# Kernel optimization log

Measured on AMD Instinct MI355X. Metric: run time of the kernel, lower is better.

Reference implementation:

```python
import jax, jax.numpy as jnp
import numpy as np

GROUPS = 32
NUM_HEADS = 4
EPS = 1e-5


def setup_inputs() -> dict:
    key = jax.random.key(0)
    ks = jax.random.split(key, 3)
    B, C, H, W = 16, 256, 32, 32
    x = jax.random.normal(ks[0], (B, C, H, W), dtype=jnp.float32)
    gn_w = jnp.ones((C,), jnp.float32)
    gn_b = jnp.zeros((C,), jnp.float32)
    qkv_w = jax.random.normal(ks[1], (3 * C, C), dtype=jnp.float32) * (1.0 / np.sqrt(C))
    qkv_b = jnp.zeros((3 * C,), jnp.float32)
    proj_w = jax.random.normal(ks[2], (C, C), dtype=jnp.float32) * (1.0 / np.sqrt(C))
    proj_b = jnp.zeros((C,), jnp.float32)
    return {"x": x, "gn_w": gn_w, "gn_b": gn_b, "qkv_w": qkv_w, "qkv_b": qkv_b,
            "proj_w": proj_w, "proj_b": proj_b}


def reference(x, gn_w, gn_b, qkv_w, qkv_b, proj_w, proj_b):
    B, C, H, W = x.shape
    N = H * W
    nh = NUM_HEADS
    hd = C // nh
    # GroupNorm(32, C)
    xg = x.reshape(B, GROUPS, C // GROUPS, N)
    mean = xg.mean(axis=(2, 3), keepdims=True)
    var = xg.var(axis=(2, 3), keepdims=True)
    xn = ((xg - mean) * jax.lax.rsqrt(var + EPS)).reshape(B, C, N)
    xn = xn * gn_w[None, :, None] + gn_b[None, :, None]
    # 1x1 conv -> qkv over spatial tokens
    qkv = jnp.einsum('oc,bcn->bon', qkv_w, xn) + qkv_b[None, :, None]
    qkv = qkv.reshape(B, 3, nh, hd, N)
    q, k, v = qkv[:, 0], qkv[:, 1], qkv[:, 2]
    scale = hd ** (-0.5)
    attn = jnp.einsum('bhdi,bhdj->bhij', q, k) * scale
    attn = jax.nn.softmax(attn, axis=-1)
    out = jnp.einsum('bhij,bhdj->bhdi', attn, v).reshape(B, C, N)
    out = jnp.einsum('oc,bcn->bon', proj_w, out) + proj_b[None, :, None]
    return x + out.reshape(B, C, H, W)
```

## Files before the change

### kernel.cpp

```cpp
#include <hip/hip_runtime.h>
#include <math.h>

#define B_   16
#define C_   256
#define N_   1024
#define NH   4
#define HD   64
#define EPSV 1e-5f
#define LOG2E 1.44269504088896f

typedef __attribute__((ext_vector_type(8)))  short  bf16x8;
typedef __attribute__((ext_vector_type(8)))  ushort us8;
typedef __attribute__((ext_vector_type(4)))  float  f32x4;
typedef __attribute__((ext_vector_type(16))) float  f32x16;

__device__ inline ushort f2bf(float f) {
    union { float f; unsigned u; } v; v.f = f;
    unsigned r = v.u + 0x7fffu + ((v.u >> 16) & 1u);
    return (ushort)(r >> 16);
}

__device__ inline unsigned cvtpk(float lo, float hi) {
    unsigned r;
    asm("v_cvt_pk_bf16_f32 %0, %1, %2" : "=v"(r) : "v"(lo), "v"(hi));
    return r;
}

__device__ inline float fexp2(float x) {
    float r;
    asm("v_exp_f32 %0, %1" : "=v"(r) : "v"(x));
    return r;
}

#if __has_builtin(__builtin_amdgcn_permlane32_swap)
__device__ inline void plswap_pair(unsigned &d, unsigned &s) {
    auto r = __builtin_amdgcn_permlane32_swap(d, s, false, false);
    d = r[0]; s = r[1];
}
__device__ inline void plswap_same(unsigned x, unsigned &lo, unsigned &hi) {
    auto r = __builtin_amdgcn_permlane32_swap(x, x, false, false);
    lo = r[0]; hi = r[1];
}
#else
__device__ inline void plswap_pair(unsigned &d, unsigned &s) {
    asm("v_permlane32_swap_b32 %0, %1" : "+v"(d), "+v"(s));
}
__device__ inline void plswap_same(unsigned x, unsigned &lo, unsigned &hi) {
    asm("v_mov_b32 %0, %2\n\t"
        "v_mov_b32 %1, %2\n\t"
        "v_permlane32_swap_b32 %0, %1"
        : "=&v"(lo), "=&v"(hi) : "v"(x));
}
#endif

__device__ inline float sumhalves(float x) {
    union { float f; unsigned u; } a; a.f = x;
    unsigned lo, hi;
    plswap_same(a.u, lo, hi);
    union { unsigned u; float f; } L, H; L.u = lo; H.u = hi;
    return L.f + H.f;
}

#define GLOAD16(gsrc, ldst) \
  __builtin_amdgcn_global_load_lds((const __attribute__((address_space(1))) unsigned int*)(gsrc), \
                                   (__attribute__((address_space(3))) unsigned int*)(ldst), 16, 0, 0)

__global__ __launch_bounds__(256) void prep_w(const float* __restrict__ qw,
                                              const float* __restrict__ pw,
                                              ushort* __restrict__ wq,
                                              ushort* __restrict__ wp) {
    int i = blockIdx.x * 256 + threadIdx.x;
    int T = gridDim.x * 256;
    for (int t = i; t < 49152; t += T) {
        float4 v = ((const float4*)qw)[t];
        ushort4 o; o.x = f2bf(v.x); o.y = f2bf(v.y); o.z = f2bf(v.z); o.w = f2bf(v.w);
        ((ushort4*)wq)[t] = o;
    }
    for (int t = i; t < 16384; t += T) {
        float4 v = ((const float4*)pw)[t];
        ushort4 o; o.x = f2bf(v.x); o.y = f2bf(v.y); o.z = f2bf(v.z); o.w = f2bf(v.w);
        ((ushort4*)wp)[t] = o;
    }
}

__global__ __launch_bounds__(256) void gn_kernel(const float* __restrict__ x,
                                                 const float* __restrict__ gw,
                                                 const float* __restrict__ gb,
                                                 ushort* __restrict__ xnt) {
    __shared__ ushort Ls[16][1028];
    __shared__ float redS[2][4], redQ[2][4], stats[2][2];
    int b = blockIdx.x >> 4, gp = blockIdx.x & 15;
    const float4* px4 = (const float4*)(x + ((size_t)b * C_ + gp * 16) * N_);
    int tid = threadIdx.x;

    float4 vals[16];
    float s0 = 0.f, q0 = 0.f, s1 = 0.f, q1 = 0.f;
    #pragma unroll
    for (int p = 0; p < 16; ++p) {
        float4 v = px4[p * 256 + tid];
        vals[p] = v;
        float ss = v.x + v.y + v.z + v.w;
        float qq = v.x * v.x + v.y * v.y + v.z * v.z + v.w * v.w;
        if (p < 8) { s0 += ss; q0 += qq; } else { s1 += ss; q1 += qq; }
    }
    #pragma unroll
    for (int off = 32; off; off >>= 1) {
        s0 += __shfl_down(s0, off); q0 += __shfl_down(q0, off);
        s1 += __shfl_down(s1, off); q1 += __shfl_down(q1, off);
    }
    int w = tid >> 6, lane = tid & 63;
    if (lane == 0) { redS[0][w] = s0; redQ[0][w] = q0; redS[1][w] = s1; redQ[1][w] = q1; }
    __syncthreads();
    if (tid < 2) {
        float S = redS[tid][0] + redS[tid][1] + redS[tid][2] + redS[tid][3];
        float Q = redQ[tid][0] + redQ[tid][1] + redQ[tid][2] + redQ[tid][3];
        float mean = S * (1.f / 8192.f);
        float var  = Q * (1.f / 8192.f) - mean * mean;
        stats[tid][0] = mean;
        stats[tid][1] = rsqrtf(var + EPSV);
    }
    __syncthreads();
    #pragma unroll
    for (int p = 0; p < 16; ++p) {
        int grp = p >> 3;
        int ch = gp * 16 + p;
        float ga = gw[ch] * stats[grp][1];
        float be = gb[ch] - stats[grp][0] * ga;
        float4 v = vals[p];
        ushort4 o;
        o.x = f2bf(v.x * ga + be); o.y = f2bf(v.y * ga + be);
        o.z = f2bf(v.z * ga + be); o.w = f2bf(v.w * ga + be);
        *(ushort4*)&Ls[p][tid * 4] = o;
    }
    __syncthreads();
    #pragma unroll
    for (int it = 0; it < 4; ++it) {
        int n = it * 256 + tid;
        us8 a, b2;
        #pragma unroll
        for (int c = 0; c < 8; ++c) { a[c] = Ls[c][n]; b2[c] = Ls[8 + c][n]; }
        ushort* dst = xnt + ((size_t)b * N_ + n) * C_ + gp * 16;
        *(us8*)dst = a;
        *(us8*)(dst + 8) = b2;
    }
}

__global__ __launch_bounds__(256) void qkv_gemm(const ushort* __restrict__ wq,
                                                const ushort* __restrict__ xnt,
                                                const float* __restrict__ bias,
                                                ushort* __restrict__ Qd,
                                                ushort* __restrict__ Kd,
                                                ushort* __restrict__ Vd) {
    __shared__ union {
        struct { ushort As[64][72]; ushort Bs[128][72]; } s;
        ushort Ts[128][72];
    } u;
    int b = blockIdx.z, mt = blockIdx.y, n0 = blockIdx.x * 128;
    int s_ = mt >> 2, h = mt & 3;
    const ushort* Bsrc = xnt + (size_t)b * N_ * C_;
    int tid = threadIdx.x;
    int w = tid >> 6, lane = tid & 63;
    int g = lane >> 4, r16 = lane & 15;
    int wm = w >> 1, wn = w & 1;

    f32x4 acc[2][4];
    #pragma unroll
    for (int mf = 0; mf < 2; ++mf)
        #pragma unroll
        for (int nf = 0; nf < 4; ++nf) acc[mf][nf] = (f32x4){0.f, 0.f, 0.f, 0.f};

    for (int k0 = 0; k0 < 256; k0 += 64) {
        __syncthreads();
        #pragma unroll
        for (int it = 0; it < 2; ++it) {
            int t = it * 256 + tid, r = t >> 3, c = t & 7;
            *(us8*)&u.s.As[r][c * 8] = *(const us8*)(wq + (size_t)(mt * 64 + r) * 256 + k0 + c * 8);
        }
        #pragma unroll
        for (int it = 0; it < 4; ++it) {
            int t = it * 256 + tid, r = t >> 3, c = t & 7;
            *(us8*)&u.s.Bs[r][c * 8] = *(const us8*)(Bsrc + (size_t)(n0 + r) * 256 + k0 + c * 8);
        }
        __syncthreads();
        bf16x8 aA[2][2], bB[4][2];
        #pragma unroll
        for (int mf = 0; mf < 2; ++mf)
            #pragma unroll
            for (int ks = 0; ks < 2; ++ks)
                aA[mf][ks] = *(const bf16x8*)&u.s.As[wm * 32 + mf * 16 + r16][ks * 32 + g * 8];
        #pragma unroll
        for (int nf = 0; nf < 4; ++nf)
            #pragma unroll
            for (int ks = 0; ks < 2; ++ks)
                bB[nf][ks] = *(const bf16x8*)&u.s.Bs[wn * 64 + nf * 16 + r16][ks * 32 + g * 8];
        #pragma unroll
        for (int ks = 0; ks < 2; ++ks)
            #pragma unroll
            for (int mf = 0; mf < 2; ++mf)
                #pragma unroll
                for (int nf = 0; nf < 4; ++nf)
                    acc[mf][nf] = __builtin_amdgcn_mfma_f32_16x16x32_bf16(aA[mf][ks], bB[nf][ks], acc[mf][nf], 0, 0, 0);
    }
    __syncthreads();

    float scale = (s_ == 0) ? 0.125f * LOG2E : 1.f;
    float bfr[2][4];
    #pragma unroll
    for (int mf = 0; mf < 2; ++mf)
        #pragma unroll
        for (int reg = 0; reg < 4; ++reg)
            bfr[mf][reg] = bias[mt * 64 + wm * 32 + mf * 16 + g * 4 + reg];

    if (s_ < 2) {
        #pragma unroll
        for (int mf = 0; mf < 2; ++mf)
            #pragma unroll
            for (int nf = 0; nf < 4; ++nf)
                #pragma unroll
                for (int reg = 0; reg < 4; ++reg)
                    u.Ts[wn * 64 + nf * 16 + r16][wm * 32 + mf * 16 + g * 4 + reg] =
                        f2bf((acc[mf][nf][reg] + bfr[mf][reg]) * scale);
        __syncthreads();
        ushort* dst = (s_ == 0 ? Qd : Kd) + ((size_t)(b * NH + h) * N_ + n0) * HD;
        #pragma unroll
        for (int it = 0; it < 4; ++it) {
            int t = it * 256 + tid, r = t >> 3, c = t & 7;
            *(us8*)(dst + (size_t)r * HD + c * 8) = *(const us8*)&u.Ts[r][c * 8];
        }
    } else {
        #pragma unroll
        for (int mf = 0; mf < 2; ++mf)
            #pragma unroll
            for (int nf = 0; nf < 4; ++nf)
                #pragma unroll
                for (int reg = 0; reg < 4; ++reg) {
                    int d = wm * 32 + mf * 16 + g * 4 + reg;
                    int n = n0 + wn * 64 + nf * 16 + r16;
                    Vd[((size_t)(b * NH + h) * HD + d) * N_ + n] = f2bf(acc[mf][nf][reg] + bfr[mf][reg]);
                }
    }
}

__global__ __launch_bounds__(128) void attn_mfma(const ushort* __restrict__ Qd,
                                                 const ushort* __restrict__ Kd,
                                                 const ushort* __restrict__ Vd,
                                                 ushort* __restrict__ att) {
    __shared__ union {
        struct { ushort Kb[2][2048]; ushort Vb[2][2048]; } s;
        float Op[64][68];
    } u;
    __shared__ float Lsh[64];
    int nblk = blockIdx.x;
    int bh = nblk & 63, qt = nblk >> 6;
    int b = bh >> 2, head = bh & 3;
    int i0 = qt * 64;
    const ushort* qp = Qd + (size_t)bh * N_ * HD;
    const ushort* kp = Kd + (size_t)bh * N_ * HD;
    const ushort* vp = Vd + (size_t)bh * HD * N_;

    int tid = threadIdx.x;
    int w = tid >> 6, lane = tid & 63;
    int hl = lane >> 5, r32 = lane & 31;

    int goff[4];
    #pragma unroll
    for (int p = 0; p < 4; ++p) {
        if (w == 0) goff[p] = r32 * HD + p * 16 + hl * 8;
        else        goff[p] = ((p & 1) * 32 + r32) * N_ + (p >> 1) * 16 + hl * 8;
    }
    const ushort* gsp = (w == 0) ? kp : vp;
    int gstep = (w == 0) ? 32 * HD : 32;

    const ushort* kbL = &u.s.Kb[0][0] + lane * 8;
    const ushort* vbL = &u.s.Vb[0][0] + lane * 8;

    bf16x8 aQ[4];
    {
        const ushort* qrow = qp + (size_t)(i0 + w * 32 + r32) * HD;
        #pragma unroll
        for (int c = 0; c < 4; ++c)
            aQ[c] = *(const bf16x8*)(qrow + c * 16 + hl * 8);
    }

    float l = 0.f;
    f32x16 oacc[2];
    #pragma unroll
    for (int dt = 0; dt < 2; ++dt)
        #pragma unroll
        for (int i = 0; i < 16; ++i) oacc[dt][i] = 0.f;

    {
        ushort* db = (w == 0) ? &u.s.Kb[0][0] : &u.s.Vb[0][0];
        #pragma unroll
        for (int p = 0; p < 4; ++p)
            GLOAD16(gsp + goff[p], db + p * 512);
    }
    __syncthreads();

    auto body = [&](int cb, int it) {
        if (it < 31) {
            const ushort* gsi = gsp + (it + 1) * gstep;
            ushort* db = (w == 0) ? &u.s.Kb[cb ^ 1][0] : &u.s.Vb[cb ^ 1][0];
            #pragma unroll
            for (int p = 0; p < 4; ++p)
                GLOAD16(gsi + goff[p], db + p * 512);
        }

        f32x16 sacc;
        #pragma unroll
        for (int i = 0; i < 16; ++i) sacc[i] = 0.f;
        __builtin_amdgcn_s_setprio(1);
        #pragma unroll
        for (int c = 0; c < 4; ++c) {
            bf16x8 aK = *(const bf16x8*)(kbL + cb * 2048 + c * 512);
            sacc = __builtin_amdgcn_mfma_f32_32x32x16_bf16(aK, aQ[c], sacc, 0, 0, 0);
        }
        __builtin_amdgcn_s_setprio(0);

        float p0[16];
        #pragma unroll
        for (int i = 0; i < 16; ++i) p0[i] = fexp2(sacc[i]);
        float s4a = (p0[0] + p0[4]) + (p0[8] + p0[12]);
        float s4b = (p0[1] + p0[5]) + (p0[9] + p0[13]);
        float s4c = (p0[2] + p0[6]) + (p0[10] + p0[14]);
        float s4d = (p0[3] + p0[7]) + (p0[11] + p0[15]);
        float sum = (s4a + s4b) + (s4c + s4d);
        sum = sumhalves(sum);
        l += sum;

        unsigned pk[4][2];
        #pragma unroll
        for (int R = 0; R < 4; ++R) {
            pk[R][0] = cvtpk(p0[R * 4 + 0], p0[R * 4 + 1]);
            pk[R][1] = cvtpk(p0[R * 4 + 2], p0[R * 4 + 3]);
        }
        unsigned apk[2][4];
        #pragma unroll
        for (int kt = 0; kt < 2; ++kt) {
            unsigned w0 = pk[2 * kt][0], w1 = pk[2 * kt][1];
            unsigned w2 = pk[2 * kt + 1][0], w3 = pk[2 * kt + 1][1];
            plswap_pair(w0, w2);
            plswap_pair(w1, w3);
            apk[kt][0] = w0; apk[kt][1] = w1;
            apk[kt][2] = w2; apk[kt][3] = w3;
        }

        __builtin_amdgcn_s_setprio(1);
        #pragma unroll
        for (int kt = 0; kt < 2; ++kt) {
            union { unsigned uu[4]; bf16x8 v; } ap;
            ap.uu[0] = apk[kt][0]; ap.uu[1] = apk[kt][1];
            ap.uu[2] = apk[kt][2]; ap.uu[3] = apk[kt][3];
            #pragma unroll
            for (int dt = 0; dt < 2; ++dt) {
                bf16x8 bV = *(const bf16x8*)(vbL + cb * 2048 + (kt * 2 + dt) * 512);
                oacc[dt] = __builtin_amdgcn_mfma_f32_32x32x16_bf16(ap.v, bV, oacc[dt], 0, 0, 0);
            }
        }
        __builtin_amdgcn_s_setprio(0);

        __syncthreads();
    };

    #pragma unroll 1
    for (int ii = 0; ii < 16; ++ii) {
        body(0, 2 * ii);
        body(1, 2 * ii + 1);
    }

    if (hl == 0) Lsh[w * 32 + r32] = 1.f / l;
    #pragma unroll
    for (int dt = 0; dt < 2; ++dt)
        #pragma unroll
        for (int reg = 0; reg < 16; ++reg)
            u.Op[w * 32 + (reg & 3) + 8 * (reg >> 2) + 4 * hl][dt * 32 + r32] = oacc[dt][reg];
    __syncthreads();

    #pragma unroll
    for (int it = 0; it < 4; ++it) {
        int t = it * 128 + tid;
        int r = t >> 3, c = t & 7;
        float linv = Lsh[r];
        f32x4 v0 = *(const f32x4*)&u.Op[r][c * 8];
        f32x4 v1 = *(const f32x4*)&u.Op[r][c * 8 + 4];
        union { unsigned uu[4]; us8 v; } ov;
        ov.uu[0] = cvtpk(v0[0] * linv, v0[1] * linv);
        ov.uu[1] = cvtpk(v0[2] * linv, v0[3] * linv);
        ov.uu[2] = cvtpk(v1[0] * linv, v1[1] * linv);
        ov.uu[3] = cvtpk(v1[2] * linv, v1[3] * linv);
        *(us8*)(att + ((size_t)b * N_ + i0 + r) * C_ + head * HD + c * 8) = ov.v;
    }
}

__global__ __launch_bounds__(256) void proj_gemm(const ushort* __restrict__ wp,
                                                 const ushort* __restrict__ att,
                                                 const float* __restrict__ bias,
                                                 const float* __restrict__ x,
                                                 float* __restrict__ out) {
    __shared__ struct { ushort As[64][72]; ushort Bs[128][72]; } s;
    int b = blockIdx.z, m0 = blockIdx.y * 64, n0 = blockIdx.x * 128;
    const ushort* Bsrc = att + (size_t)b * N_ * C_;
    int tid = threadIdx.x;
    int w = tid >> 6, lane = tid & 63;
    int g = lane >> 4, r16 = lane & 15;
    int wm = w >> 1, wn = w & 1;

    f32x4 acc[2][4];
    #pragma unroll
    for (int mf = 0; mf < 2; ++mf)
        #pragma unroll
        for (int nf = 0; nf < 4; ++nf) acc[mf][nf] = (f32x4){0.f, 0.f, 0.f, 0.f};

    for (int k0 = 0; k0 < 256; k0 += 64) {
        __syncthreads();
        #pragma unroll
        for (int it = 0; it < 2; ++it) {
            int t = it * 256 + tid, r = t >> 3, c = t & 7;
            *(us8*)&s.As[r][c * 8] = *(const us8*)(wp + (size_t)(m0 + r) * 256 + k0 + c * 8);
        }
        #pragma unroll
        for (int it = 0; it < 4; ++it) {
            int t = it * 256 + tid, r = t >> 3, c = t & 7;
            *(us8*)&s.Bs[r][c * 8] = *(const us8*)(Bsrc + (size_t)(n0 + r) * 256 + k0 + c * 8);
        }
        __syncthreads();
        bf16x8 aA[2][2], bB[4][2];
        #pragma unroll
        for (int mf = 0; mf < 2; ++mf)
            #pragma unroll
            for (int ks = 0; ks < 2; ++ks)
                aA[mf][ks] = *(const bf16x8*)&s.As[wm * 32 + mf * 16 + r16][ks * 32 + g * 8];
        #pragma unroll
        for (int nf = 0; nf < 4; ++nf)
            #pragma unroll
            for (int ks = 0; ks < 2; ++ks)
                bB[nf][ks] = *(const bf16x8*)&s.Bs[wn * 64 + nf * 16 + r16][ks * 32 + g * 8];
        #pragma unroll
        for (int ks = 0; ks < 2; ++ks)
            #pragma unroll
            for (int mf = 0; mf < 2; ++mf)
                #pragma unroll
                for (int nf = 0; nf < 4; ++nf)
                    acc[mf][nf] = __builtin_amdgcn_mfma_f32_16x16x32_bf16(aA[mf][ks], bB[nf][ks], acc[mf][nf], 0, 0, 0);
    }

    #pragma unroll
    for (int mf = 0; mf < 2; ++mf) {
        #pragma unroll
        for (int reg = 0; reg < 4; ++reg) {
            int c_ = m0 + wm * 32 + mf * 16 + g * 4 + reg;
            float bi = bias[c_];
            #pragma unroll
            for (int nf = 0; nf < 4; ++nf) {
                int n = n0 + wn * 64 + nf * 16 + r16;
                size_t o = ((size_t)b * C_ + c_) * N_ + n;
                out[o] = acc[mf][nf][reg] + bi + x[o];
            }
        }
    }
}

extern "C" void kernel_launch(void* const* d_in, const int* in_sizes, int n_in,
                              void* d_out, int out_size, void* d_ws, size_t ws_size,
                              hipStream_t stream) {
    const float* x      = (const float*)d_in[0];
    const float* gn_w   = (const float*)d_in[1];
    const float* gn_b   = (const float*)d_in[2];
    const float* qkv_w  = (const float*)d_in[3];
    const float* qkv_b  = (const float*)d_in[4];
    const float* proj_w = (const float*)d_in[5];
    const float* proj_b = (const float*)d_in[6];
    float* out = (float*)d_out;

    char* ws = (char*)d_ws;
    ushort* wq_bf = (ushort*)(ws);
    ushort* wp_bf = (ushort*)(ws + 393216);
    ushort* xnt   = (ushort*)(ws + (1u << 20));
    ushort* Qd    = (ushort*)(ws + (size_t)16 * 1024 * 1024);
    ushort* Kd    = (ushort*)(ws + (size_t)24 * 1024 * 1024);
    ushort* Vd    = (ushort*)(ws + (size_t)32 * 1024 * 1024);
    ushort* att_t = (ushort*)(ws + (size_t)40 * 1024 * 1024);

    prep_w<<<dim3(256), dim3(256), 0, stream>>>(qkv_w, proj_w, wq_bf, wp_bf);
    gn_kernel<<<dim3(B_ * 16), dim3(256), 0, stream>>>(x, gn_w, gn_b, xnt);
    qkv_gemm<<<dim3(8, 12, B_), dim3(256), 0, stream>>>(wq_bf, xnt, qkv_b, Qd, Kd, Vd);
    attn_mfma<<<dim3(1024), dim3(128), 0, stream>>>(Qd, Kd, Vd, att_t);
    proj_gemm<<<dim3(8, 4, B_), dim3(256), 0, stream>>>(wp_bf, att_t, proj_b, x, out);
}
```

Baseline: 75.09 us.

## Split the KV sequence across two wave pairs in the attention kernel

Doubles the attention block to 256 threads. Two wave pairs each stream half of the K/V sequence into their own double-buffered shared memory and run half as many loop iterations. Their partial softmax denominators and output accumulators are then summed through shared memory before normalisation. This aims to shorten the serial per-block KV loop and put more waves on each CU, at the cost of more shared memory per block and an extra reduction step with a barrier. The merge is only correct if both halves use the same softmax reference value.

```diff
diff --git a/kernel.cpp b/kernel.cpp
--- a/kernel.cpp
+++ b/kernel.cpp
@@ -241,12 +241,12 @@
     }
 }
 
-__global__ __launch_bounds__(128) void attn_mfma(const ushort* __restrict__ Qd,
+__global__ __launch_bounds__(256) void attn_mfma(const ushort* __restrict__ Qd,
                                                  const ushort* __restrict__ Kd,
                                                  const ushort* __restrict__ Vd,
                                                  ushort* __restrict__ att) {
     __shared__ union {
-        struct { ushort Kb[2][2048]; ushort Vb[2][2048]; } s;
+        struct { ushort Kb[2][2][2048]; ushort Vb[2][2][2048]; } s;
         float Op[64][68];
     } u;
     __shared__ float Lsh[64];
@@ -260,23 +260,24 @@
 
     int tid = threadIdx.x;
     int w = tid >> 6, lane = tid & 63;
+    int pair = w >> 1, w01 = w & 1;
     int hl = lane >> 5, r32 = lane & 31;
 
     int goff[4];
     #pragma unroll
     for (int p = 0; p < 4; ++p) {
-        if (w == 0) goff[p] = r32 * HD + p * 16 + hl * 8;
-        else        goff[p] = ((p & 1) * 32 + r32) * N_ + (p >> 1) * 16 + hl * 8;
-    }
-    const ushort* gsp = (w == 0) ? kp : vp;
-    int gstep = (w == 0) ? 32 * HD : 32;
-
-    const ushort* kbL = &u.s.Kb[0][0] + lane * 8;
-    const ushort* vbL = &u.s.Vb[0][0] + lane * 8;
+        if (w01 == 0) goff[p] = r32 * HD + p * 16 + hl * 8;
+        else          goff[p] = ((p & 1) * 32 + r32) * N_ + (p >> 1) * 16 + hl * 8;
+    }
+    const ushort* gsp = (w01 == 0) ? (kp + (size_t)pair * 512 * HD) : (vp + pair * 512);
+    int gstep = (w01 == 0) ? 32 * HD : 32;
+
+    const ushort* kbL = &u.s.Kb[pair][0][0] + lane * 8;
+    const ushort* vbL = &u.s.Vb[pair][0][0] + lane * 8;
 
     bf16x8 aQ[4];
     {
-        const ushort* qrow = qp + (size_t)(i0 + w * 32 + r32) * HD;
+        const ushort* qrow = qp + (size_t)(i0 + w01 * 32 + r32) * HD;
         #pragma unroll
         for (int c = 0; c < 4; ++c)
             aQ[c] = *(const bf16x8*)(qrow + c * 16 + hl * 8);
@@ -290,7 +291,7 @@
         for (int i = 0; i < 16; ++i) oacc[dt][i] = 0.f;
 
     {
-        ushort* db = (w == 0) ? &u.s.Kb[0][0] : &u.s.Vb[0][0];
+        ushort* db = (w01 == 0) ? &u.s.Kb[pair][0][0] : &u.s.Vb[pair][0][0];
         #pragma unroll
         for (int p = 0; p < 4; ++p)
             GLOAD16(gsp + goff[p], db + p * 512);
@@ -298,9 +299,9 @@
     __syncthreads();
 
     auto body = [&](int cb, int it) {
-        if (it < 31) {
+        if (it < 15) {
             const ushort* gsi = gsp + (it + 1) * gstep;
-            ushort* db = (w == 0) ? &u.s.Kb[cb ^ 1][0] : &u.s.Vb[cb ^ 1][0];
+            ushort* db = (w01 == 0) ? &u.s.Kb[pair][cb ^ 1][0] : &u.s.Vb[pair][cb ^ 1][0];
             #pragma unroll
             for (int p = 0; p < 4; ++p)
                 GLOAD16(gsi + goff[p], db + p * 512);
@@ -363,24 +364,35 @@
     };
 
     #pragma unroll 1
-    for (int ii = 0; ii < 16; ++ii) {
+    for (int ii = 0; ii < 8; ++ii) {
         body(0, 2 * ii);
         body(1, 2 * ii + 1);
     }
 
-    if (hl == 0) Lsh[w * 32 + r32] = 1.f / l;
-    #pragma unroll
-    for (int dt = 0; dt < 2; ++dt)
-        #pragma unroll
-        for (int reg = 0; reg < 16; ++reg)
-            u.Op[w * 32 + (reg & 3) + 8 * (reg >> 2) + 4 * hl][dt * 32 + r32] = oacc[dt][reg];
-    __syncthreads();
-
-    #pragma unroll
-    for (int it = 0; it < 4; ++it) {
-        int t = it * 128 + tid;
+    if (pair == 0) {
+        if (hl == 0) Lsh[w01 * 32 + r32] = l;
+        #pragma unroll
+        for (int dt = 0; dt < 2; ++dt)
+            #pragma unroll
+            for (int reg = 0; reg < 16; ++reg)
+                u.Op[w01 * 32 + (reg & 3) + 8 * (reg >> 2) + 4 * hl][dt * 32 + r32] = oacc[dt][reg];
+    }
+    __syncthreads();
+    if (pair == 1) {
+        if (hl == 0) Lsh[w01 * 32 + r32] += l;
+        #pragma unroll
+        for (int dt = 0; dt < 2; ++dt)
+            #pragma unroll
+            for (int reg = 0; reg < 16; ++reg)
+                u.Op[w01 * 32 + (reg & 3) + 8 * (reg >> 2) + 4 * hl][dt * 32 + r32] += oacc[dt][reg];
+    }
+    __syncthreads();
+
+    #pragma unroll
+    for (int it = 0; it < 2; ++it) {
+        int t = it * 256 + tid;
         int r = t >> 3, c = t & 7;
-        float linv = Lsh[r];
+        float linv = 1.f / Lsh[r];
         f32x4 v0 = *(const f32x4*)&u.Op[r][c * 8];
         f32x4 v1 = *(const f32x4*)&u.Op[r][c * 8 + 4];
         union { unsigned uu[4]; us8 v; } ov;
@@ -484,6 +496,6 @@
     prep_w<<<dim3(256), dim3(256), 0, stream>>>(qkv_w, proj_w, wq_bf, wp_bf);
     gn_kernel<<<dim3(B_ * 16), dim3(256), 0, stream>>>(x, gn_w, gn_b, xnt);
     qkv_gemm<<<dim3(8, 12, B_), dim3(256), 0, stream>>>(wq_bf, xnt, qkv_b, Qd, Kd, Vd);
-    attn_mfma<<<dim3(1024), dim3(128), 0, stream>>>(Qd, Kd, Vd, att_t);
+    attn_mfma<<<dim3(1024), dim3(256), 0, stream>>>(Qd, Kd, Vd, att_t);
     proj_gemm<<<dim3(8, 4, B_), dim3(256), 0, stream>>>(wp_bf, att_t, proj_b, x, out);
 }
```

Result: slower. 83.03 us (+10.6%).

## Give each wave private K/V buffers and drop per-iteration block barriers

Applied to the files above, without the earlier changes.

The attention kernel previously had wave 0 load K tiles and wave 1 load V tiles into shared buffers, which forced a __syncthreads after every key block. Now each wave loads its own copy of both K and V into a private double buffer and waits only on its own vmcnt, so the per-iteration barrier is removed. This doubles the global-to-LDS traffic per block and the LDS footprint of the staging buffers. The gain depends on barrier stalls outweighing the duplicated loads.

```diff
diff --git a/kernel.cpp b/kernel.cpp
--- a/kernel.cpp
+++ b/kernel.cpp
@@ -64,6 +64,11 @@
 #define GLOAD16(gsrc, ldst) \
   __builtin_amdgcn_global_load_lds((const __attribute__((address_space(1))) unsigned int*)(gsrc), \
                                    (__attribute__((address_space(3))) unsigned int*)(ldst), 16, 0, 0)
+
+#define WAITVM(N) do { \
+    asm volatile("s_waitcnt vmcnt(" #N ")" ::: "memory"); \
+    __builtin_amdgcn_sched_barrier(0); \
+} while (0)
 
 __global__ __launch_bounds__(256) void prep_w(const float* __restrict__ qw,
                                               const float* __restrict__ pw,
@@ -246,7 +251,7 @@
                                                  const ushort* __restrict__ Vd,
                                                  ushort* __restrict__ att) {
     __shared__ union {
-        struct { ushort Kb[2][2048]; ushort Vb[2][2048]; } s;
+        ushort B[2][2][2][2048];
         float Op[64][68];
     } u;
     __shared__ float Lsh[64];
@@ -262,17 +267,14 @@
     int w = tid >> 6, lane = tid & 63;
     int hl = lane >> 5, r32 = lane & 31;
 
-    int goff[4];
+    int kgoff[4], vgoff[4];
     #pragma unroll
     for (int p = 0; p < 4; ++p) {
-        if (w == 0) goff[p] = r32 * HD + p * 16 + hl * 8;
-        else        goff[p] = ((p & 1) * 32 + r32) * N_ + (p >> 1) * 16 + hl * 8;
-    }
-    const ushort* gsp = (w == 0) ? kp : vp;
-    int gstep = (w == 0) ? 32 * HD : 32;
-
-    const ushort* kbL = &u.s.Kb[0][0] + lane * 8;
-    const ushort* vbL = &u.s.Vb[0][0] + lane * 8;
+        kgoff[p] = r32 * HD + p * 16 + hl * 8;
+        vgoff[p] = ((p & 1) * 32 + r32) * N_ + (p >> 1) * 16 + hl * 8;
+    }
+    const ushort* kbL = &u.B[w][0][0][0] + lane * 8;
+    const ushort* vbL = &u.B[w][0][1][0] + lane * 8;
 
     bf16x8 aQ[4];
     {
@@ -289,21 +291,24 @@
         #pragma unroll
         for (int i = 0; i < 16; ++i) oacc[dt][i] = 0.f;
 
-    {
-        ushort* db = (w == 0) ? &u.s.Kb[0][0] : &u.s.Vb[0][0];
-        #pragma unroll
-        for (int p = 0; p < 4; ++p)
-            GLOAD16(gsp + goff[p], db + p * 512);
-    }
-    __syncthreads();
+    #pragma unroll
+    for (int p = 0; p < 4; ++p) {
+        GLOAD16(kp + kgoff[p], &u.B[w][0][0][p * 512]);
+        GLOAD16(vp + vgoff[p], &u.B[w][0][1][p * 512]);
+    }
 
     auto body = [&](int cb, int it) {
         if (it < 31) {
-            const ushort* gsi = gsp + (it + 1) * gstep;
-            ushort* db = (w == 0) ? &u.s.Kb[cb ^ 1][0] : &u.s.Vb[cb ^ 1][0];
-            #pragma unroll
-            for (int p = 0; p < 4; ++p)
-                GLOAD16(gsi + goff[p], db + p * 512);
+            const ushort* kpi = kp + (it + 1) * (32 * HD);
+            const ushort* vpi = vp + (it + 1) * 32;
+            #pragma unroll
+            for (int p = 0; p < 4; ++p) {
+                GLOAD16(kpi + kgoff[p], &u.B[w][cb ^ 1][0][p * 512]);
+                GLOAD16(vpi + vgoff[p], &u.B[w][cb ^ 1][1][p * 512]);
+            }
+            WAITVM(8);
+        } else {
+            WAITVM(0);
         }
 
         f32x16 sacc;
@@ -312,7 +317,7 @@
         __builtin_amdgcn_s_setprio(1);
         #pragma unroll
         for (int c = 0; c < 4; ++c) {
-            bf16x8 aK = *(const bf16x8*)(kbL + cb * 2048 + c * 512);
+            bf16x8 aK = *(const bf16x8*)(kbL + cb * 4096 + c * 512);
             sacc = __builtin_amdgcn_mfma_f32_32x32x16_bf16(aK, aQ[c], sacc, 0, 0, 0);
         }
         __builtin_amdgcn_s_setprio(0);
@@ -353,13 +358,11 @@
             ap.uu[2] = apk[kt][2]; ap.uu[3] = apk[kt][3];
             #pragma unroll
             for (int dt = 0; dt < 2; ++dt) {
-                bf16x8 bV = *(const bf16x8*)(vbL + cb * 2048 + (kt * 2 + dt) * 512);
+                bf16x8 bV = *(const bf16x8*)(vbL + cb * 4096 + (kt * 2 + dt) * 512);
                 oacc[dt] = __builtin_amdgcn_mfma_f32_32x32x16_bf16(ap.v, bV, oacc[dt], 0, 0, 0);
             }
         }
         __builtin_amdgcn_s_setprio(0);
-
-        __syncthreads();
     };
 
     #pragma unroll 1
@@ -368,6 +371,7 @@
         body(1, 2 * ii + 1);
     }
 
+    __syncthreads();
     if (hl == 0) Lsh[w * 32 + r32] = 1.f / l;
     #pragma unroll
     for (int dt = 0; dt < 2; ++dt)
```

New measurement: 103.3 us. +37.6%, slower.
